# Optimization experiments

Measured on AMD Instinct MI355X. Metric: run time of the kernel, lower is better.

The kernel has to match this reference:

```python
import jax, jax.numpy as jnp
import numpy as np

B, NO, NM, NV, E = 16, 512, 128, 64, 256
H, DK, MS, FF = 16, 16, 8, 512
TRANS_MAX = 100.0


def _ln(x):
    m = x.mean(-1, keepdims=True)
    v = ((x - m) ** 2).mean(-1, keepdims=True)
    return (x - m) * jax.lax.rsqrt(v + 1e-5)


def _inv_norm(x):
    # 1 - minmax-normalize over the whole per-batch matrix
    mn = x.min(axis=(1, 2), keepdims=True)
    mx = x.max(axis=(1, 2), keepdims=True)
    return 1.0 - (x - mn) / (mx - mn)


def _adjacency(proc_time, trans_time, MVpair_trans, mask_dyn, mask_ma):
    # masked copy of proc_time
    A_proc = jnp.where(mask_dyn, proc_time, 0.0)
    # keep only the per-row minimum nonzero entry (min_ProcTime_elements)
    nz = jnp.where(A_proc == 0.0, jnp.inf, A_proc)
    mn = nz.min(axis=2, keepdims=True)
    keep = (A_proc == mn) & (A_proc != 0.0)
    A_proc = A_proc * keep.astype(proc_time.dtype)
    A_proc_norm = (A_proc > 0.0).astype(proc_time.dtype)
    # machine-machine masks
    mask2 = mask_ma[:, None, :] & mask_ma[:, :, None]  # [B, nm, nm]
    A_procing = (~mask2).astype(proc_time.dtype)
    A_off = _inv_norm(MVpair_trans)
    tt = jnp.where(mask2, trans_time, TRANS_MAX + 1.0)
    A_on = _inv_norm(tt)
    return A_proc_norm, A_procing, A_off, A_on


def _block(row, col, cost, Wq, Wk, Wv, Wo, mW1, mb1, mW2, mb2, fW1, fb1, fW2, fb2):
    # MatNet-style mixed-score multi-head attention encoding block
    Bb, R, _ = row.shape
    C = col.shape[1]
    q = (row @ Wq).reshape(Bb, R, H, DK).transpose(0, 2, 1, 3)  # bhrd
    k = (col @ Wk).reshape(Bb, C, H, DK).transpose(0, 2, 1, 3)  # bhcd
    v = (col @ Wv).reshape(Bb, C, H, DK).transpose(0, 2, 1, 3)
    dot = jnp.einsum('bhrd,bhcd->bhrc', q, k) / jnp.sqrt(jnp.asarray(DK, row.dtype))
    two = jnp.stack([dot, jnp.broadcast_to(cost[:, None], dot.shape)], axis=-1)  # [B,H,R,C,2]
    hmix = jax.nn.relu(jnp.einsum('bhrct,hts->bhrcs', two, mW1) + mb1[None, :, None, None, :])
    score = jnp.einsum('bhrcs,hso->bhrco', hmix, mW2)[..., 0] + mb2[:, 0][None, :, None, None]
    attn = jax.nn.softmax(score, axis=-1)
    ctx = jnp.einsum('bhrc,bhcd->bhrd', attn, v).transpose(0, 2, 1, 3).reshape(Bb, R, H * DK)
    out1 = _ln(row + ctx @ Wo)
    ffn = jax.nn.relu(out1 @ fW1 + fb1) @ fW2 + fb2
    return _ln(out1 + ffn)


def setup_inputs() -> dict:
    key = jax.random.key(0)
    ks = jax.random.split(key, 24)

    def nrm(i, shape, s=0.05):
        return jax.random.normal(ks[i], shape, jnp.float32) * s

    return {
        'ope_emb': nrm(0, (B, NO, E), 1.0),
        'ma_emb': nrm(1, (B, NM, E), 1.0),
        'veh_emb': nrm(2, (B, NV, E), 1.0),
        'proc_time': jax.random.uniform(ks[3], (B, NO, NM), jnp.float32) * 20.0,
        'offload_trans_time': jax.random.uniform(ks[4], (B, NO, NV), jnp.float32) * TRANS_MAX,
        'trans_time': jax.random.uniform(ks[5], (B, NM, NM), jnp.float32) * TRANS_MAX,
        'MVpair_trans': jax.random.uniform(ks[6], (B, NV, NM), jnp.float32) * TRANS_MAX,
        'mask_dyn_ope_ma_adj': jax.random.bernoulli(ks[7], 0.3, (B, NO, NM)),
        'mask_ma': jax.random.bernoulli(ks[8], 0.7, (B, NM)),
        # stacked params for the 4 blocks: 0=ope, 1=veh, 2=ma1, 3=ma2
        'Wq': nrm(9, (4, E, H * DK)),
        'Wk': nrm(10, (4, E, H * DK)),
        'Wv': nrm(11, (4, E, H * DK)),
        'Wo': nrm(12, (4, H * DK, E)),
        'mixW1': nrm(13, (4, H, 2, MS), 0.3),
        'mixb1': jnp.zeros((4, H, MS), jnp.float32),
        'mixW2': nrm(14, (4, H, MS, 1), 0.3),
        'mixb2': jnp.zeros((4, H, 1), jnp.float32),
        'ffW1': nrm(15, (4, E, FF)),
        'ffb1': jnp.zeros((4, FF), jnp.float32),
        'ffW2': nrm(16, (4, FF, E)),
        'ffb2': jnp.zeros((4, E), jnp.float32),
        'maprojW': nrm(17, (2 * E, E)),
        'maprojb': jnp.zeros((E,), jnp.float32),
    }


def reference(ope_emb, ma_emb, veh_emb, proc_time, offload_trans_time, trans_time,
              MVpair_trans, mask_dyn_ope_ma_adj, mask_ma,
              Wq, Wk, Wv, Wo, mixW1, mixb1, mixW2, mixb2,
              ffW1, ffb1, ffW2, ffb2, maprojW, maprojb):
    A_proc_norm, A_procing, A_off, A_on = _adjacency(
        proc_time, trans_time, MVpair_trans, mask_dyn_ope_ma_adj, mask_ma)

    def blk(i, row, col, cost):
        return _block(row, col, cost, Wq[i], Wk[i], Wv[i], Wo[i],
                      mixW1[i], mixb1[i], mixW2[i], mixb2[i],
                      ffW1[i], ffb1[i], ffW2[i], ffb2[i])

    ope_out = blk(0, ope_emb, ma_emb, A_proc_norm)
    veh_out = blk(1, veh_emb, ma_emb, A_off)
    ma1 = blk(2, ma_emb, ma_emb, A_procing)
    ma2 = blk(3, ma_emb, ma_emb, A_on)
    ma_out = jnp.concatenate([ma1, ma2], axis=-1) @ maprojW + maprojb
    return (ope_out, ma_out, veh_out)
```

## Files before the change

### kernel.cpp

```cpp
#include <hip/hip_runtime.h>
#include <hip/hip_fp16.h>
#include <hip/hip_bf16.h>


typedef unsigned short u16;
typedef __attribute__((ext_vector_type(8))) short bf16x8;
typedef __attribute__((ext_vector_type(4))) float f32x4;
struct us4 { u16 x, y, z, w; };

__device__ __forceinline__ float bf2f(u16 u) {
  return __uint_as_float(((unsigned int)u) << 16);
}
__device__ __forceinline__ u16 f2bf(float f) {
  unsigned int x = __float_as_uint(f);
  x += 0x7FFFu + ((x >> 16) & 1u);
  return (u16)(x >> 16);
}
__device__ __forceinline__ __half2 h2max(__half2 a, __half2 b) {
  unsigned au = *(unsigned*)&a, bu = *(unsigned*)&b, ru;
  asm("v_pk_max_f16 %0, %1, %2" : "=v"(ru) : "v"(au), "v"(bu));
  return *(__half2*)&ru;
}

#define NBATCH 16
#define NOPE   512
#define NMA    128
#define NVEH   64
#define EDIM   256

struct PrepArgs {
  const float* ope; const float* ma; const float* veh;
  u16* ope_bf; u16* ma_bf; u16* veh_bf;
  const float* proc; const int* mask_dyn; float* A_proc;
  const float* mv; const float* trans; const int* mask_ma;
  unsigned int* mm;
};
__global__ __launch_bounds__(256) void prep_a(PrepArgs a) {
  int blk = blockIdx.x, t = threadIdx.x;
  if (blk < 2816) {
    int i = blk * 256 + t;
    const float* s; u16* d; int j;
    if (i < 524288)      { s = a.ope; d = a.ope_bf; j = i; }
    else if (i < 655360) { s = a.ma;  d = a.ma_bf;  j = i - 524288; }
    else                 { s = a.veh; d = a.veh_bf; j = i - 655360; }
    float4 v = ((const float4*)s)[j];
    us4 o = { f2bf(v.x), f2bf(v.y), f2bf(v.z), f2bf(v.w) };
    ((us4*)d)[j] = o;
    return;
  }
  if (blk < 6912) {
    int local = blk - 2816;
    int row = local * 2 + (t >> 7);
    int lane = t & 127;
    size_t idx = (size_t)row * NMA + lane;
    float av = a.mask_dyn[idx] ? a.proc[idx] : 0.0f;
    float cand = (av != 0.0f) ? av : 1.0e30f;
    __shared__ float red[256];
    red[t] = cand;
    __syncthreads();
    for (int s = 64; s > 0; s >>= 1) {
      if (lane < s) red[t] = fminf(red[t], red[t + s]);
      __syncthreads();
    }
    float mn = red[t & 128];
    a.A_proc[idx] = (av != 0.0f && av == mn) ? 1.0f : 0.0f;
    return;
  }
  __shared__ float smn[256], smx[256];
  float mn = 1.0e30f, mx = -1.0e30f;
  int mmIdx;
  if (blk < 6976) {
    int local = blk - 6912;
    int b = local >> 2, chunk = local & 3;
    const float* xb = a.mv + (size_t)b * 8192 + chunk * 2048;
#pragma unroll
    for (int r = 0; r < 8; r++) {
      float v = xb[r * 256 + t];
      mn = fminf(mn, v);
      mx = fmaxf(mx, v);
    }
    mmIdx = b;
  } else {
    int local = blk - 6976;
    int b = local >> 3, chunk = local & 7;
    __shared__ unsigned char mrow[NMA];
    if (t < NMA) mrow[t] = (unsigned char)(a.mask_ma[(size_t)b * NMA + t] != 0);
    __syncthreads();
    const float* tb = a.trans + (size_t)b * 16384 + chunk * 2048;
    int rbase = chunk * 16;
#pragma unroll
    for (int r = 0; r < 8; r++) {
      int off = r * 256 + t;
      int row = rbase + (off >> 7), col = off & 127;
      bool m2 = mrow[row] && mrow[col];
      float tt = m2 ? tb[off] : 101.0f;
      mn = fminf(mn, tt);
      mx = fmaxf(mx, tt);
    }
    mmIdx = 16 + b;
  }
  smn[t] = mn; smx[t] = mx;
  __syncthreads();
  for (int s = 128; s > 0; s >>= 1) {
    if (t < s) {
      smn[t] = fminf(smn[t], smn[t + s]);
      smx[t] = fmaxf(smx[t], smx[t + s]);
    }
    __syncthreads();
  }
  if (t == 0) {
    atomicMin(&a.mm[mmIdx], __float_as_uint(smn[0]));
    atomicMax(&a.mm[32 + mmIdx], __float_as_uint(smx[0]));
  }
}

__global__ __launch_bounds__(256) void prep_b(
    const float* __restrict__ mv, const float* __restrict__ trans,
    const int* __restrict__ mask_ma, const unsigned int* __restrict__ mm,
    float* __restrict__ A_offb, float* __restrict__ a_on,
    float* __restrict__ a_pcing) {
  int blk = blockIdx.x, t = threadIdx.x;
  if (blk < 512) {
    int b = blk >> 5, off = (blk & 31) * 256 + t;
    float lo = __uint_as_float(mm[b]);
    float inv = 1.0f / (__uint_as_float(mm[32 + b]) - lo);
    size_t idx = (size_t)b * 8192 + off;
    A_offb[idx] = 1.0f - (mv[idx] - lo) * inv;
    return;
  }
  int local = blk - 512;
  int b = local >> 6, off = (local & 63) * 256 + t;
  int row = off >> 7, col = off & 127;
  bool m2 = (mask_ma[(size_t)b * NMA + row] != 0) &&
            (mask_ma[(size_t)b * NMA + col] != 0);
  size_t idx = (size_t)b * 16384 + off;
  float tt = m2 ? trans[idx] : 101.0f;
  float lo = __uint_as_float(mm[16 + b]);
  float inv = 1.0f / (__uint_as_float(mm[48 + b]) - lo);
  a_on[idx] = 1.0f - (tt - lo) * inv;
  a_pcing[idx] = m2 ? 0.0f : 1.0f;
}

struct TrArgs {
  const float* Wq; const float* Wk; const float* Wv; const float* Wo;
  const float* ffW1; const float* ffW2; const float* maproj;
  u16* WqT; u16* WkT; u16* WvT; u16* WoT; u16* ffW1T; u16* ffW2T; u16* maprojT;
};
__global__ __launch_bounds__(256) void transpose_all(TrArgs a) {
  int blk = blockIdx.x;
  const float* src; u16* dst; int Kd, Nd, tile;
  if (blk < 1024) {
    int w = blk >> 8, i = (blk >> 6) & 3; tile = blk & 63;
    const float* sw = (w == 0 ? a.Wq : w == 1 ? a.Wk : w == 2 ? a.Wv : a.Wo);
    u16* dw = (w == 0 ? a.WqT : w == 1 ? a.WkT : w == 2 ? a.WvT : a.WoT);
    src = sw + (size_t)i * 65536; dst = dw + (size_t)i * 65536;
    Kd = 256; Nd = 256;
  } else if (blk < 1536) {
    int z = (blk - 1024) >> 7; tile = (blk - 1024) & 127;
    src = a.ffW1 + (size_t)z * 131072; dst = a.ffW1T + (size_t)z * 131072;
    Kd = 256; Nd = 512;
  } else {
    int z = (blk - 1536) >> 7; tile = (blk - 1536) & 127;
    if (z < 4) { src = a.ffW2 + (size_t)z * 131072; dst = a.ffW2T + (size_t)z * 131072; }
    else       { src = a.maproj; dst = a.maprojT; }
    Kd = 512; Nd = 256;
  }
  int nx = Nd >> 5;
  int k0 = (tile / nx) * 32, n0 = (tile % nx) * 32;
  __shared__ float tl[32][33];
  int tx = threadIdx.x & 31, ty = threadIdx.x >> 5;
#pragma unroll
  for (int r = 0; r < 4; r++)
    tl[ty + r * 8][tx] = src[(size_t)(k0 + ty + r * 8) * Nd + n0 + tx];
  __syncthreads();
#pragma unroll
  for (int r = 0; r < 4; r++)
    dst[(size_t)(n0 + ty + r * 8) * Kd + k0 + tx] = f2bf(tl[tx][ty + r * 8]);
}

__global__ __launch_bounds__(256) void transpose_v(
    const u16* __restrict__ src, u16* __restrict__ dst) {
  int g = blockIdx.z >> 4, b = blockIdx.z & 15;
  int d0 = blockIdx.x * 32, c0 = blockIdx.y * 32;
  __shared__ u16 tile[32][33];
  int tx = threadIdx.x & 31, ty = threadIdx.x >> 5;
  const u16* s = src + ((size_t)g * 16 + b) * 32768;
  u16* d = dst + ((size_t)g * 16 + b) * 32768;
#pragma unroll
  for (int r = 0; r < 4; r++)
    tile[ty + r * 8][tx] = s[(size_t)(c0 + ty + r * 8) * 256 + d0 + tx];
  __syncthreads();
#pragma unroll
  for (int r = 0; r < 4; r++)
    d[(size_t)(d0 + ty + r * 8) * 128 + c0 + tx] = tile[tx][ty + r * 8];
}

struct GG {
  const u16* A; const u16* WT; const float* bias; u16* C;
  int M, N, K, epi, wgStart, wgCols, mode;
};
struct GGArgs { GG g[12]; int n; };

__global__ __launch_bounds__(256) void gemm_grouped(GGArgs args) {
  int wg = blockIdx.x;
  int gi = 0;
  for (int i = 1; i < args.n; i++)
    if (wg >= args.g[i].wgStart) gi = i;
  GG gg = args.g[gi];
  int lwg = wg - gg.wgStart;
  int bx = lwg & (gg.wgCols - 1);
  int by = lwg >> ((gg.wgCols == 2) ? 1 : 2);
  int N = gg.N, K = gg.K;

  __shared__ u16 As[128][40];
  __shared__ u16 Bs[128][40];
  int tid = threadIdx.x;
  int lane = tid & 63, wid = tid >> 6;
  int wr = (wid >> 1) * 64, wc = (wid & 1) * 64;
  int m16 = lane & 15, quad = lane >> 4;
  int rb = by * 128, cb = bx * 128;
  int srow = tid >> 2;
  int schunk = (tid & 3) * 8;

  f32x4 acc[4][4];
#pragma unroll
  for (int i = 0; i < 4; i++)
#pragma unroll
    for (int j = 0; j < 4; j++) acc[i][j] = (f32x4){0.f, 0.f, 0.f, 0.f};

  for (int k0 = 0; k0 < K; k0 += 32) {
    uint4 va0 = *(const uint4*)(gg.A + (size_t)(rb + srow) * K + k0 + schunk);
    uint4 va1 = *(const uint4*)(gg.A + (size_t)(rb + 64 + srow) * K + k0 + schunk);
    uint4 vb0 = *(const uint4*)(gg.WT + (size_t)(cb + srow) * K + k0 + schunk);
    uint4 vb1 = *(const uint4*)(gg.WT + (size_t)(cb + 64 + srow) * K + k0 + schunk);
    __syncthreads();
    *(uint4*)&As[srow][schunk] = va0;
    *(uint4*)&As[64 + srow][schunk] = va1;
    *(uint4*)&Bs[srow][schunk] = vb0;
    *(uint4*)&Bs[64 + srow][schunk] = vb1;
    __syncthreads();
    bf16x8 af[4], bfr[4];
#pragma unroll
    for (int i = 0; i < 4; i++)
      af[i] = *(const bf16x8*)&As[wr + i * 16 + m16][quad * 8];
#pragma unroll
    for (int j = 0; j < 4; j++)
      bfr[j] = *(const bf16x8*)&Bs[wc + j * 16 + m16][quad * 8];
#pragma unroll
    for (int i = 0; i < 4; i++)
#pragma unroll
      for (int j = 0; j < 4; j++)
        acc[i][j] = __builtin_amdgcn_mfma_f32_16x16x32_bf16(
            af[i], bfr[j], acc[i][j], 0, 0, 0);
  }

#pragma unroll
  for (int i = 0; i < 4; i++) {
#pragma unroll
    for (int j = 0; j < 4; j++) {
      int col = cb + wc + j * 16 + m16;
      float bv = (gg.epi >= 1) ? gg.bias[col] : 0.0f;
#pragma unroll
      for (int r = 0; r < 4; r++) {
        int row = rb + wr + i * 16 + quad * 4 + r;
        float v = acc[i][j][r] + bv;
        if (gg.epi == 2) v = fmaxf(v, 0.0f);
        size_t off;
        if (gg.mode == 0) {
          off = (size_t)row * N + col;
        } else if (gg.mode == 1) {
          off = ((size_t)(row >> 4)) * 4096 + (size_t)(col >> 4) * 256 +
                (size_t)(row & 15) * 16 + (col & 15);
        } else {
          off = ((size_t)(row >> 7)) * 32768 + (size_t)(col >> 4) * 2048 +
                (size_t)(row & 127) * 16 + (col & 15);
        }
        gg.C[off] = f2bf(v);
      }
    }
  }
}

__global__ __launch_bounds__(256) void gemm_mfma_f32(
    const u16* __restrict__ A, const u16* __restrict__ WT,
    const float* __restrict__ bias, float* __restrict__ C,
    int M, int N, int K) {
  __shared__ u16 As[128][40];
  __shared__ u16 Bs[128][40];
  int tid = threadIdx.x;
  int lane = tid & 63, wid = tid >> 6;
  int wr = (wid >> 1) * 64, wc = (wid & 1) * 64;
  int m16 = lane & 15, quad = lane >> 4;
  int rb = blockIdx.y * 128, cb = blockIdx.x * 128;
  int srow = tid >> 2;
  int schunk = (tid & 3) * 8;
  f32x4 acc[4][4];
#pragma unroll
  for (int i = 0; i < 4; i++)
#pragma unroll
    for (int j = 0; j < 4; j++) acc[i][j] = (f32x4){0.f, 0.f, 0.f, 0.f};
  for (int k0 = 0; k0 < K; k0 += 32) {
    uint4 va0 = *(const uint4*)(A + (size_t)(rb + srow) * K + k0 + schunk);
    uint4 va1 = *(const uint4*)(A + (size_t)(rb + 64 + srow) * K + k0 + schunk);
    uint4 vb0 = *(const uint4*)(WT + (size_t)(cb + srow) * K + k0 + schunk);
    uint4 vb1 = *(const uint4*)(WT + (size_t)(cb + 64 + srow) * K + k0 + schunk);
    __syncthreads();
    *(uint4*)&As[srow][schunk] = va0;
    *(uint4*)&As[64 + srow][schunk] = va1;
    *(uint4*)&Bs[srow][schunk] = vb0;
    *(uint4*)&Bs[64 + srow][schunk] = vb1;
    __syncthreads();
    bf16x8 af[4], bfr[4];
#pragma unroll
    for (int i = 0; i < 4; i++)
      af[i] = *(const bf16x8*)&As[wr + i * 16 + m16][quad * 8];
#pragma unroll
    for (int j = 0; j < 4; j++)
      bfr[j] = *(const bf16x8*)&Bs[wc + j * 16 + m16][quad * 8];
#pragma unroll
    for (int i = 0; i < 4; i++)
#pragma unroll
      for (int j = 0; j < 4; j++)
        acc[i][j] = __builtin_amdgcn_mfma_f32_16x16x32_bf16(
            af[i], bfr[j], acc[i][j], 0, 0, 0);
  }
#pragma unroll
  for (int i = 0; i < 4; i++)
#pragma unroll
    for (int j = 0; j < 4; j++) {
      int col = cb + wc + j * 16 + m16;
      float bv = bias[col];
#pragma unroll
      for (int r = 0; r < 4; r++) {
        int row = rb + wr + i * 16 + quad * 4 + r;
        C[(size_t)row * N + col] = acc[i][j][r] + bv;
      }
    }
}

struct AG {
  const u16* q; const u16* k; const u16* vT; const float* cost; u16* ctx;
  const float* w1; const float* b1; const float* w2; const float* b2;
  int R, wgStart;
};
struct AGArgs { AG g[4]; };

#define CSTRIDE 134

__global__ __launch_bounds__(256) void attn_grouped(AGArgs args) {
  int blk = blockIdx.x;
  int gi = 0;
#pragma unroll
  for (int i = 1; i < 4; i++)
    if (blk >= args.g[i].wgStart) gi = i;
  AG gg = args.g[gi];
  int local = blk - gg.wgStart;

  int t = threadIdx.x;
  int wave = t >> 6, lane = t & 63;
  int quad = lane >> 4, l16 = lane & 15;
  int j = local & 15;
  int b = (j & 7) * 2 + (j >> 3);
  int hgrp = (local >> 4) & 1;
  int tile = local >> 5;
  int m0 = b * gg.R + tile * 16;

  __shared__ __half costs_h[16 * CSTRIDE];
  __shared__ u16 pbuf[4][16 * 136];

  const float* cp = gg.cost + (size_t)m0 * 128;
  for (int i = t; i < 2048; i += 256)
    costs_h[(i >> 7) * CSTRIDE + (i & 127)] = __float2half(cp[i]);
  __syncthreads();

  const bf16x8 zerof = (bf16x8){0, 0, 0, 0, 0, 0, 0, 0};
  const f32x4 zacc = (f32x4){0.f, 0.f, 0.f, 0.f};
  const __half2 zh = __float2half2_rn(0.0f);
  u16* pb = pbuf[wave];
  const u16* qtile = gg.q + ((size_t)(m0 >> 4)) * 4096;
  const u16* kb    = gg.k + (size_t)b * 32768;

#pragma unroll
  for (int hh = 0; hh < 2; hh++) {
    int h = hgrp * 8 + wave * 2 + hh;

    __half2 w10h[8], w11h[8], b1h[8], w2h[8];
#pragma unroll
    for (int s = 0; s < 8; s++) {
      w10h[s] = __float2half2_rn(gg.w1[h * 16 + s] * 0.25f);
      w11h[s] = __float2half2_rn(gg.w1[h * 16 + 8 + s]);
      b1h[s]  = __float2half2_rn(gg.b1[h * 8 + s]);
      w2h[s]  = __float2half2_rn(gg.w2[h * 8 + s]);
    }
    float wb2v = gg.b2[h];

    bf16x8 bq = zerof;
    if (quad < 2)
      bq = *(const bf16x8*)(qtile + (size_t)h * 256 + l16 * 16 + quad * 8);
    f32x4 st[8];
#pragma unroll
    for (int ct = 0; ct < 8; ct++) {
      bf16x8 ak = zerof;
      if (quad < 2)
        ak = *(const bf16x8*)(kb + (size_t)h * 2048 + (ct * 16 + l16) * 16 +
                              quad * 8);
      st[ct] = __builtin_amdgcn_mfma_f32_16x16x32_bf16(ak, bq, zacc, 0, 0, 0);
    }

#pragma unroll
    for (int ct = 0; ct < 8; ct++) {
#pragma unroll
      for (int p = 0; p < 2; p++) {
        __half2 d2 = __float22half2_rn(
            make_float2(st[ct][p * 2], st[ct][p * 2 + 1]));
        __half2 c2 = *(const __half2*)&costs_h[l16 * CSTRIDE + ct * 16 +
                                               quad * 4 + p * 2];
        __half2 s2 = zh;
#pragma unroll
        for (int s = 0; s < 8; s++) {
          __half2 hm = __hfma2(d2, w10h[s], __hfma2(c2, w11h[s], b1h[s]));
          hm = h2max(hm, zh);
          s2 = __hfma2(hm, w2h[s], s2);
        }
        float2 sf = __half22float2(s2);
        st[ct][p * 2]     = sf.x + wb2v;
        st[ct][p * 2 + 1] = sf.y + wb2v;
      }
    }

    float mx = -1.0e30f;
#pragma unroll
    for (int ct = 0; ct < 8; ct++)
#pragma unroll
      for (int rg = 0; rg < 4; rg++) mx = fmaxf(mx, st[ct][rg]);
    mx = fmaxf(mx, __shfl_xor(mx, 16, 64));
    mx = fmaxf(mx, __shfl_xor(mx, 32, 64));
    float sum = 0.0f;
#pragma unroll
    for (int ct = 0; ct < 8; ct++)
#pragma unroll
      for (int rg = 0; rg < 4; rg++) {
        float e = __expf(st[ct][rg] - mx);
        st[ct][rg] = e;
        sum += e;
      }
    sum += __shfl_xor(sum, 16, 64);
    sum += __shfl_xor(sum, 32, 64);
    float inv = 1.0f / sum;

#pragma unroll
    for (int ct = 0; ct < 8; ct++) {
#pragma unroll
      for (int p = 0; p < 2; p++) {
        __hip_bfloat162 pk = __float22bfloat162_rn(
            make_float2(st[ct][p * 2] * inv, st[ct][p * 2 + 1] * inv));
        *(unsigned int*)&pb[l16 * 136 + ct * 16 + quad * 4 + p * 2] =
            *(unsigned int*)&pk;
      }
    }

    f32x4 cacc = zacc;
#pragma unroll
    for (int ks = 0; ks < 4; ks++) {
      bf16x8 ap = *(const bf16x8*)&pb[l16 * 136 + ks * 32 + quad * 8];
      bf16x8 bv = *(const bf16x8*)(gg.vT + (size_t)b * 32768 +
                                   (size_t)(h * 16 + l16) * 128 + ks * 32 +
                                   quad * 8);
      cacc = __builtin_amdgcn_mfma_f32_16x16x32_bf16(ap, bv, cacc, 0, 0, 0);
    }

#pragma unroll
    for (int rg = 0; rg < 4; rg++)
      gg.ctx[(size_t)(m0 + quad * 4 + rg) * 256 + h * 16 + l16] =
          f2bf(cacc[rg]);
  }
}

struct LN1Args {
  const float* r0; const float* r1; const float* r2; const float* r3;
  int s1, s2, s3;
};
__global__ __launch_bounds__(256) void ln1_grouped(
    LN1Args a, const u16* __restrict__ x, u16* __restrict__ out) {
  int row = blockIdx.x, t = threadIdx.x;
  const float* resid;
  int local;
  if (row < a.s1)      { resid = a.r0; local = row; }
  else if (row < a.s2) { resid = a.r1; local = row - a.s1; }
  else if (row < a.s3) { resid = a.r2; local = row - a.s2; }
  else                 { resid = a.r3; local = row - a.s3; }
  float vv = resid[(size_t)local * 256 + t] + bf2f(x[(size_t)row * 256 + t]);
  __shared__ float red[256];
  red[t] = vv;
  __syncthreads();
  for (int s = 128; s > 0; s >>= 1) {
    if (t < s) red[t] += red[t + s];
    __syncthreads();
  }
  float mean = red[0] * (1.0f / 256.0f);
  __syncthreads();
  float d = vv - mean;
  red[t] = d * d;
  __syncthreads();
  for (int s = 128; s > 0; s >>= 1) {
    if (t < s) red[t] += red[t + s];
    __syncthreads();
  }
  float var = red[0] * (1.0f / 256.0f);
  out[(size_t)row * 256 + t] = f2bf(d * rsqrtf(var + 1e-5f));
}

struct LN2Args {
  float* f0; float* f1; u16* b2; u16* b3;
  int s1, s2, s3;
};
__global__ __launch_bounds__(256) void ln2_grouped(
    LN2Args a, const u16* __restrict__ resid, const u16* __restrict__ x) {
  int row = blockIdx.x, t = threadIdx.x;
  float vv = bf2f(resid[(size_t)row * 256 + t]) + bf2f(x[(size_t)row * 256 + t]);
  __shared__ float red[256];
  red[t] = vv;
  __syncthreads();
  for (int s = 128; s > 0; s >>= 1) {
    if (t < s) red[t] += red[t + s];
    __syncthreads();
  }
  float mean = red[0] * (1.0f / 256.0f);
  __syncthreads();
  float d = vv - mean;
  red[t] = d * d;
  __syncthreads();
  for (int s = 128; s > 0; s >>= 1) {
    if (t < s) red[t] += red[t + s];
    __syncthreads();
  }
  float var = red[0] * (1.0f / 256.0f);
  float y = d * rsqrtf(var + 1e-5f);
  if (row < a.s1)
    a.f0[(size_t)row * 256 + t] = y;
  else if (row < a.s2)
    a.f1[(size_t)(row - a.s1) * 256 + t] = y;
  else if (row < a.s3)
    a.b2[(size_t)(row - a.s2) * 512 + t] = f2bf(y);
  else
    a.b3[(size_t)(row - a.s3) * 512 + 256 + t] = f2bf(y);
}

extern "C" void kernel_launch(void* const* d_in, const int* in_sizes, int n_in,
                              void* d_out, int out_size, void* d_ws, size_t ws_size,
                              hipStream_t stream) {
  const float* ope   = (const float*)d_in[0];
  const float* ma    = (const float*)d_in[1];
  const float* veh   = (const float*)d_in[2];
  const float* proc  = (const float*)d_in[3];
  const float* trans = (const float*)d_in[5];
  const float* mv    = (const float*)d_in[6];
  const int* mask_dyn = (const int*)d_in[7];
  const int* mask_ma  = (const int*)d_in[8];
  const float* Wq = (const float*)d_in[9];
  const float* Wk = (const float*)d_in[10];
  const float* Wv = (const float*)d_in[11];
  const float* Wo = (const float*)d_in[12];
  const float* mixW1 = (const float*)d_in[13];
  const float* mixb1 = (const float*)d_in[14];
  const float* mixW2 = (const float*)d_in[15];
  const float* mixb2 = (const float*)d_in[16];
  const float* ffW1 = (const float*)d_in[17];
  const float* ffb1 = (const float*)d_in[18];
  const float* ffW2 = (const float*)d_in[19];
  const float* ffb2 = (const float*)d_in[20];
  const float* maprojW = (const float*)d_in[21];
  const float* maprojb = (const float*)d_in[22];
  float* out = (float*)d_out;
  char* ws = (char*)d_ws;

  const int OFF[4] = {0, 8192, 9216, 11264};
  const int MS4[4] = {8192, 1024, 2048, 2048};
  const int TOT = 13312;

  const size_t MB = 1 << 20;
  float* A_proc  = (float*)(ws + 0);
  float* A_offb  = (float*)(ws + 4 * MB);
  float* A_pcing = (float*)(ws + 4 * MB + MB / 2);
  float* A_on    = (float*)(ws + 5 * MB + MB / 2);
  u16* ope_bf  = (u16*)(ws + 6 * MB + MB / 2);
  u16* ma_bf   = (u16*)(ws + 10 * MB + MB / 2);
  u16* veh_bf  = (u16*)(ws + 11 * MB + MB / 2);
  u16* WqT     = (u16*)(ws + 12 * MB);
  u16* WkT     = (u16*)(ws + 12 * MB + MB / 2);
  u16* WvT     = (u16*)(ws + 13 * MB);
  u16* WoT     = (u16*)(ws + 13 * MB + MB / 2);
  u16* ffW1T   = (u16*)(ws + 14 * MB);
  u16* ffW2T   = (u16*)(ws + 15 * MB);
  u16* maprojT = (u16*)(ws + 16 * MB);
  u16* q_all   = (u16*)(ws + 16 * MB + MB / 2);
  u16* k_all   = (u16*)(ws + 23 * MB);
  u16* v_all   = (u16*)(ws + 27 * MB);
  u16* vT_all  = (u16*)(ws + 31 * MB);
  u16* ctx_all = (u16*)(ws + 35 * MB);
  u16* t1_all  = (u16*)(ws + 41 * MB + MB / 2);
  u16* out1_all= (u16*)(ws + 48 * MB);
  u16* ffh_all = (u16*)(ws + 54 * MB + MB / 2);
  u16* maCat   = (u16*)(ws + 67 * MB + MB / 2);
  unsigned int* mmbuf = (unsigned int*)(ws + 70 * MB);

  hipMemsetAsync(mmbuf, 0x7F, 128, stream);
  hipMemsetAsync((char*)mmbuf + 128, 0x00, 128, stream);

  {
    PrepArgs pa = {ope, ma, veh, ope_bf, ma_bf, veh_bf,
                   proc, mask_dyn, A_proc, mv, trans, mask_ma, mmbuf};
    prep_a<<<7104, 256, 0, stream>>>(pa);
  }

  {
    TrArgs ta = {Wq, Wk, Wv, Wo, ffW1, ffW2, maprojW,
                 WqT, WkT, WvT, WoT, ffW1T, ffW2T, maprojT};
    transpose_all<<<2176, 256, 0, stream>>>(ta);
  }

  prep_b<<<1536, 256, 0, stream>>>(mv, trans, mask_ma, mmbuf,
                                   A_offb, A_on, A_pcing);

  const size_t MA_OUT  = (size_t)NBATCH * NOPE * EDIM;
  const size_t VEH_OUT = MA_OUT + (size_t)NBATCH * NMA * EDIM;

  const u16* rowbf[4] = {ope_bf, veh_bf, ma_bf, ma_bf};
  const float* costp[4] = {A_proc, A_offb, A_pcing, A_on};

  {
    GGArgs ga; ga.n = 12;
    int wg = 0;
    for (int i = 0; i < 4; i++) {
      ga.g[i] = {rowbf[i], WqT + (size_t)i * 65536, nullptr,
                 q_all + (size_t)OFF[i] * 256, MS4[i], 256, 256, 0, wg, 2, 1};
      wg += (MS4[i] / 128) * 2;
    }
    for (int i = 0; i < 4; i++) {
      ga.g[4 + i] = {ma_bf, WkT + (size_t)i * 65536, nullptr,
                     k_all + (size_t)i * 524288, 2048, 256, 256, 0, wg, 2, 2};
      wg += 32;
    }
    for (int i = 0; i < 4; i++) {
      ga.g[8 + i] = {ma_bf, WvT + (size_t)i * 65536, nullptr,
                     v_all + (size_t)i * 524288, 2048, 256, 256, 0, wg, 2, 0};
      wg += 32;
    }
    gemm_grouped<<<wg, 256, 0, stream>>>(ga);
  }

  transpose_v<<<dim3(8, 4, 64), 256, 0, stream>>>(v_all, vT_all);

  {
    AGArgs aa;
    int wg = 0;
    const int R4[4] = {NOPE, NVEH, NMA, NMA};
    for (int i = 0; i < 4; i++) {
      aa.g[i] = {q_all + (size_t)OFF[i] * 256, k_all + (size_t)i * 524288,
                 vT_all + (size_t)i * 524288, costp[i],
                 ctx_all + (size_t)OFF[i] * 256,
                 mixW1 + (size_t)i * 256, mixb1 + (size_t)i * 128,
                 mixW2 + (size_t)i * 128, mixb2 + (size_t)i * 16,
                 R4[i], wg};
      wg += MS4[i] / 8;
    }
    attn_grouped<<<wg, 256, 0, stream>>>(aa);
  }

  {
    GGArgs ga; ga.n = 4;
    int wg = 0;
    for (int i = 0; i < 4; i++) {
      ga.g[i] = {ctx_all + (size_t)OFF[i] * 256, WoT + (size_t)i * 65536,
                 nullptr, t1_all + (size_t)OFF[i] * 256,
                 MS4[i], 256, 256, 0, wg, 2, 0};
      wg += (MS4[i] / 128) * 2;
    }
    gemm_grouped<<<wg, 256, 0, stream>>>(ga);
  }

  {
    LN1Args la = {ope, veh, ma, ma, 8192, 9216, 11264};
    ln1_grouped<<<TOT, 256, 0, stream>>>(la, t1_all, out1_all);
  }

  {
    GGArgs ga; ga.n = 4;
    int wg = 0;
    for (int i = 0; i < 4; i++) {
      ga.g[i] = {out1_all + (size_t)OFF[i] * 256, ffW1T + (size_t)i * 131072,
                 ffb1 + (size_t)i * 512, ffh_all + (size_t)OFF[i] * 512,
                 MS4[i], 512, 256, 2, wg, 4, 0};
      wg += (MS4[i] / 128) * 4;
    }
    gemm_grouped<<<wg, 256, 0, stream>>>(ga);
  }

  {
    GGArgs ga; ga.n = 4;
    int wg = 0;
    for (int i = 0; i < 4; i++) {
      ga.g[i] = {ffh_all + (size_t)OFF[i] * 512, ffW2T + (size_t)i * 131072,
                 ffb2 + (size_t)i * 256, t1_all + (size_t)OFF[i] * 256,
                 MS4[i], 256, 512, 1, wg, 2, 0};
      wg += (MS4[i] / 128) * 2;
    }
    gemm_grouped<<<wg, 256, 0, stream>>>(ga);
  }

  {
    LN2Args la = {out, out + VEH_OUT, maCat, maCat, 8192, 9216, 11264};
    ln2_grouped<<<TOT, 256, 0, stream>>>(la, out1_all, t1_all);
  }

  gemm_mfma_f32<<<dim3(2, 16), 256, 0, stream>>>(maCat, maprojT, maprojb,
      out + MA_OUT, 2048, 256, 512);
}
```

Before: 279.2 us.

## Fuse weight transpose into prep, warp-level layernorm, smaller final GEMM tiles, MFMA priority

Folds the weight-transpose kernel into the prep kernel as extra blocks, which removes one launch. Both layernorm kernels now use one 64-lane wave per row with vectorized loads and shuffle reductions instead of shared-memory tree reductions. Variance is now computed in a single pass as E[x^2]-mean^2, which adds a small numerical risk. The final projection GEMM moves from 128x128 to 64x64 tiles to put more workgroups on the GPU, and s_setprio is raised around the MFMA loops in attention.

```diff
diff --git a/kernel.cpp b/kernel.cpp
--- a/kernel.cpp
+++ b/kernel.cpp
@@ -35,7 +35,12 @@
   const float* mv; const float* trans; const int* mask_ma;
   unsigned int* mm;
 };
-__global__ __launch_bounds__(256) void prep_a(PrepArgs a) {
+struct TrArgs {
+  const float* Wq; const float* Wk; const float* Wv; const float* Wo;
+  const float* ffW1; const float* ffW2; const float* maproj;
+  u16* WqT; u16* WkT; u16* WvT; u16* WoT; u16* ffW1T; u16* ffW2T; u16* maprojT;
+};
+__global__ __launch_bounds__(256) void prep_a(PrepArgs a, TrArgs tr) {
   int blk = blockIdx.x, t = threadIdx.x;
   if (blk < 2816) {
     int i = blk * 256 + t;
@@ -66,51 +71,85 @@
     a.A_proc[idx] = (av != 0.0f && av == mn) ? 1.0f : 0.0f;
     return;
   }
-  __shared__ float smn[256], smx[256];
-  float mn = 1.0e30f, mx = -1.0e30f;
-  int mmIdx;
-  if (blk < 6976) {
-    int local = blk - 6912;
-    int b = local >> 2, chunk = local & 3;
-    const float* xb = a.mv + (size_t)b * 8192 + chunk * 2048;
-#pragma unroll
-    for (int r = 0; r < 8; r++) {
-      float v = xb[r * 256 + t];
-      mn = fminf(mn, v);
-      mx = fmaxf(mx, v);
-    }
-    mmIdx = b;
-  } else {
-    int local = blk - 6976;
-    int b = local >> 3, chunk = local & 7;
-    __shared__ unsigned char mrow[NMA];
-    if (t < NMA) mrow[t] = (unsigned char)(a.mask_ma[(size_t)b * NMA + t] != 0);
+  if (blk < 7104) {
+    __shared__ float smn[256], smx[256];
+    float mn = 1.0e30f, mx = -1.0e30f;
+    int mmIdx;
+    if (blk < 6976) {
+      int local = blk - 6912;
+      int b = local >> 2, chunk = local & 3;
+      const float* xb = a.mv + (size_t)b * 8192 + chunk * 2048;
+#pragma unroll
+      for (int r = 0; r < 8; r++) {
+        float v = xb[r * 256 + t];
+        mn = fminf(mn, v);
+        mx = fmaxf(mx, v);
+      }
+      mmIdx = b;
+    } else {
+      int local = blk - 6976;
+      int b = local >> 3, chunk = local & 7;
+      __shared__ unsigned char mrow[NMA];
+      if (t < NMA) mrow[t] = (unsigned char)(a.mask_ma[(size_t)b * NMA + t] != 0);
+      __syncthreads();
+      const float* tb = a.trans + (size_t)b * 16384 + chunk * 2048;
+      int rbase = chunk * 16;
+#pragma unroll
+      for (int r = 0; r < 8; r++) {
+        int off = r * 256 + t;
+        int row = rbase + (off >> 7), col = off & 127;
+        bool m2 = mrow[row] && mrow[col];
+        float tt = m2 ? tb[off] : 101.0f;
+        mn = fminf(mn, tt);
+        mx = fmaxf(mx, tt);
+      }
+      mmIdx = 16 + b;
+    }
+    smn[t] = mn; smx[t] = mx;
     __syncthreads();
-    const float* tb = a.trans + (size_t)b * 16384 + chunk * 2048;
-    int rbase = chunk * 16;
-#pragma unroll
-    for (int r = 0; r < 8; r++) {
-      int off = r * 256 + t;
-      int row = rbase + (off >> 7), col = off & 127;
-      bool m2 = mrow[row] && mrow[col];
-      float tt = m2 ? tb[off] : 101.0f;
-      mn = fminf(mn, tt);
-      mx = fmaxf(mx, tt);
-    }
-    mmIdx = 16 + b;
-  }
-  smn[t] = mn; smx[t] = mx;
-  __syncthreads();
-  for (int s = 128; s > 0; s >>= 1) {
-    if (t < s) {
-      smn[t] = fminf(smn[t], smn[t + s]);
-      smx[t] = fmaxf(smx[t], smx[t + s]);
-    }
+    for (int s = 128; s > 0; s >>= 1) {
+      if (t < s) {
+        smn[t] = fminf(smn[t], smn[t + s]);
+        smx[t] = fmaxf(smx[t], smx[t + s]);
+      }
+      __syncthreads();
+    }
+    if (t == 0) {
+      atomicMin(&a.mm[mmIdx], __float_as_uint(smn[0]));
+      atomicMax(&a.mm[32 + mmIdx], __float_as_uint(smx[0]));
+    }
+    return;
+  }
+  {
+    int b2 = blk - 7104;
+    const float* src; u16* dst; int Kd, Nd, tile;
+    if (b2 < 1024) {
+      int w = b2 >> 8, i = (b2 >> 6) & 3; tile = b2 & 63;
+      const float* sw = (w == 0 ? tr.Wq : w == 1 ? tr.Wk : w == 2 ? tr.Wv : tr.Wo);
+      u16* dw = (w == 0 ? tr.WqT : w == 1 ? tr.WkT : w == 2 ? tr.WvT : tr.WoT);
+      src = sw + (size_t)i * 65536; dst = dw + (size_t)i * 65536;
+      Kd = 256; Nd = 256;
+    } else if (b2 < 1536) {
+      int z = (b2 - 1024) >> 7; tile = (b2 - 1024) & 127;
+      src = tr.ffW1 + (size_t)z * 131072; dst = tr.ffW1T + (size_t)z * 131072;
+      Kd = 256; Nd = 512;
+    } else {
+      int z = (b2 - 1536) >> 7; tile = (b2 - 1536) & 127;
+      if (z < 4) { src = tr.ffW2 + (size_t)z * 131072; dst = tr.ffW2T + (size_t)z * 131072; }
+      else       { src = tr.maproj; dst = tr.maprojT; }
+      Kd = 512; Nd = 256;
+    }
+    int nx = Nd >> 5;
+    int k0 = (tile / nx) * 32, n0 = (tile % nx) * 32;
+    __shared__ float tl[32][33];
+    int tx = t & 31, ty = t >> 5;
+#pragma unroll
+    for (int r = 0; r < 4; r++)
+      tl[ty + r * 8][tx] = src[(size_t)(k0 + ty + r * 8) * Nd + n0 + tx];
     __syncthreads();
-  }
-  if (t == 0) {
-    atomicMin(&a.mm[mmIdx], __float_as_uint(smn[0]));
-    atomicMax(&a.mm[32 + mmIdx], __float_as_uint(smx[0]));
+#pragma unroll
+    for (int r = 0; r < 4; r++)
+      dst[(size_t)(n0 + ty + r * 8) * Kd + k0 + tx] = f2bf(tl[tx][ty + r * 8]);
   }
 }
 
@@ -139,43 +178,6 @@
   float inv = 1.0f / (__uint_as_float(mm[48 + b]) - lo);
   a_on[idx] = 1.0f - (tt - lo) * inv;
   a_pcing[idx] = m2 ? 0.0f : 1.0f;
-}
-
-struct TrArgs {
-  const float* Wq; const float* Wk; const float* Wv; const float* Wo;
-  const float* ffW1; const float* ffW2; const float* maproj;
-  u16* WqT; u16* WkT; u16* WvT; u16* WoT; u16* ffW1T; u16* ffW2T; u16* maprojT;
-};
-__global__ __launch_bounds__(256) void transpose_all(TrArgs a) {
-  int blk = blockIdx.x;
-  const float* src; u16* dst; int Kd, Nd, tile;
-  if (blk < 1024) {
-    int w = blk >> 8, i = (blk >> 6) & 3; tile = blk & 63;
-    const float* sw = (w == 0 ? a.Wq : w == 1 ? a.Wk : w == 2 ? a.Wv : a.Wo);
-    u16* dw = (w == 0 ? a.WqT : w == 1 ? a.WkT : w == 2 ? a.WvT : a.WoT);
-    src = sw + (size_t)i * 65536; dst = dw + (size_t)i * 65536;
-    Kd = 256; Nd = 256;
-  } else if (blk < 1536) {
-    int z = (blk - 1024) >> 7; tile = (blk - 1024) & 127;
-    src = a.ffW1 + (size_t)z * 131072; dst = a.ffW1T + (size_t)z * 131072;
-    Kd = 256; Nd = 512;
-  } else {
-    int z = (blk - 1536) >> 7; tile = (blk - 1536) & 127;
-    if (z < 4) { src = a.ffW2 + (size_t)z * 131072; dst = a.ffW2T + (size_t)z * 131072; }
-    else       { src = a.maproj; dst = a.maprojT; }
-    Kd = 512; Nd = 256;
-  }
-  int nx = Nd >> 5;
-  int k0 = (tile / nx) * 32, n0 = (tile % nx) * 32;
-  __shared__ float tl[32][33];
-  int tx = threadIdx.x & 31, ty = threadIdx.x >> 5;
-#pragma unroll
-  for (int r = 0; r < 4; r++)
-    tl[ty + r * 8][tx] = src[(size_t)(k0 + ty + r * 8) * Nd + n0 + tx];
-  __syncthreads();
-#pragma unroll
-  for (int r = 0; r < 4; r++)
-    dst[(size_t)(n0 + ty + r * 8) * Kd + k0 + tx] = f2bf(tl[tx][ty + r * 8]);
 }
 
 __global__ __launch_bounds__(256) void transpose_v(
@@ -285,49 +287,45 @@
     const u16* __restrict__ A, const u16* __restrict__ WT,
     const float* __restrict__ bias, float* __restrict__ C,
     int M, int N, int K) {
-  __shared__ u16 As[128][40];
-  __shared__ u16 Bs[128][40];
+  __shared__ u16 As[64][40];
+  __shared__ u16 Bs[64][40];
   int tid = threadIdx.x;
   int lane = tid & 63, wid = tid >> 6;
-  int wr = (wid >> 1) * 64, wc = (wid & 1) * 64;
+  int wr = (wid >> 1) * 32, wc = (wid & 1) * 32;
   int m16 = lane & 15, quad = lane >> 4;
-  int rb = blockIdx.y * 128, cb = blockIdx.x * 128;
+  int rb = blockIdx.y * 64, cb = blockIdx.x * 64;
   int srow = tid >> 2;
   int schunk = (tid & 3) * 8;
-  f32x4 acc[4][4];
-#pragma unroll
-  for (int i = 0; i < 4; i++)
-#pragma unroll
-    for (int j = 0; j < 4; j++) acc[i][j] = (f32x4){0.f, 0.f, 0.f, 0.f};
+  f32x4 acc[2][2];
+#pragma unroll
+  for (int i = 0; i < 2; i++)
+#pragma unroll
+    for (int j = 0; j < 2; j++) acc[i][j] = (f32x4){0.f, 0.f, 0.f, 0.f};
   for (int k0 = 0; k0 < K; k0 += 32) {
-    uint4 va0 = *(const uint4*)(A + (size_t)(rb + srow) * K + k0 + schunk);
-    uint4 va1 = *(const uint4*)(A + (size_t)(rb + 64 + srow) * K + k0 + schunk);
-    uint4 vb0 = *(const uint4*)(WT + (size_t)(cb + srow) * K + k0 + schunk);
-    uint4 vb1 = *(const uint4*)(WT + (size_t)(cb + 64 + srow) * K + k0 + schunk);
+    uint4 va = *(const uint4*)(A + (size_t)(rb + srow) * K + k0 + schunk);
+    uint4 vb = *(const uint4*)(WT + (size_t)(cb + srow) * K + k0 + schunk);
     __syncthreads();
-    *(uint4*)&As[srow][schunk] = va0;
-    *(uint4*)&As[64 + srow][schunk] = va1;
-    *(uint4*)&Bs[srow][schunk] = vb0;
-    *(uint4*)&Bs[64 + srow][schunk] = vb1;
+    *(uint4*)&As[srow][schunk] = va;
+    *(uint4*)&Bs[srow][schunk] = vb;
     __syncthreads();
-    bf16x8 af[4], bfr[4];
-#pragma unroll
-    for (int i = 0; i < 4; i++)
+    bf16x8 af[2], bfr[2];
+#pragma unroll
+    for (int i = 0; i < 2; i++)
       af[i] = *(const bf16x8*)&As[wr + i * 16 + m16][quad * 8];
 #pragma unroll
-    for (int j = 0; j < 4; j++)
+    for (int j = 0; j < 2; j++)
       bfr[j] = *(const bf16x8*)&Bs[wc + j * 16 + m16][quad * 8];
 #pragma unroll
-    for (int i = 0; i < 4; i++)
-#pragma unroll
-      for (int j = 0; j < 4; j++)
+    for (int i = 0; i < 2; i++)
+#pragma unroll
+      for (int j = 0; j < 2; j++)
         acc[i][j] = __builtin_amdgcn_mfma_f32_16x16x32_bf16(
             af[i], bfr[j], acc[i][j], 0, 0, 0);
   }
 #pragma unroll
-  for (int i = 0; i < 4; i++)
-#pragma unroll
-    for (int j = 0; j < 4; j++) {
+  for (int i = 0; i < 2; i++)
+#pragma unroll
+    for (int j = 0; j < 2; j++) {
       int col = cb + wc + j * 16 + m16;
       float bv = bias[col];
 #pragma unroll
@@ -398,6 +396,7 @@
     if (quad < 2)
       bq = *(const bf16x8*)(qtile + (size_t)h * 256 + l16 * 16 + quad * 8);
     f32x4 st[8];
+    __builtin_amdgcn_s_setprio(1);
 #pragma unroll
     for (int ct = 0; ct < 8; ct++) {
       bf16x8 ak = zerof;
@@ -406,6 +405,7 @@
                               quad * 8);
       st[ct] = __builtin_amdgcn_mfma_f32_16x16x32_bf16(ak, bq, zacc, 0, 0, 0);
     }
+    __builtin_amdgcn_s_setprio(0);
 
 #pragma unroll
     for (int ct = 0; ct < 8; ct++) {
@@ -460,6 +460,7 @@
     }
 
     f32x4 cacc = zacc;
+    __builtin_amdgcn_s_setprio(1);
 #pragma unroll
     for (int ks = 0; ks < 4; ks++) {
       bf16x8 ap = *(const bf16x8*)&pb[l16 * 136 + ks * 32 + quad * 8];
@@ -468,6 +469,7 @@
                                    quad * 8);
       cacc = __builtin_amdgcn_mfma_f32_16x16x32_bf16(ap, bv, cacc, 0, 0, 0);
     }
+    __builtin_amdgcn_s_setprio(0);
 
 #pragma unroll
     for (int rg = 0; rg < 4; rg++)
@@ -482,32 +484,33 @@
 };
 __global__ __launch_bounds__(256) void ln1_grouped(
     LN1Args a, const u16* __restrict__ x, u16* __restrict__ out) {
-  int row = blockIdx.x, t = threadIdx.x;
+  int row = blockIdx.x * 4 + (threadIdx.x >> 6);
+  int lane = threadIdx.x & 63;
   const float* resid;
   int local;
   if (row < a.s1)      { resid = a.r0; local = row; }
   else if (row < a.s2) { resid = a.r1; local = row - a.s1; }
   else if (row < a.s3) { resid = a.r2; local = row - a.s2; }
   else                 { resid = a.r3; local = row - a.s3; }
-  float vv = resid[(size_t)local * 256 + t] + bf2f(x[(size_t)row * 256 + t]);
-  __shared__ float red[256];
-  red[t] = vv;
-  __syncthreads();
-  for (int s = 128; s > 0; s >>= 1) {
-    if (t < s) red[t] += red[t + s];
-    __syncthreads();
-  }
-  float mean = red[0] * (1.0f / 256.0f);
-  __syncthreads();
-  float d = vv - mean;
-  red[t] = d * d;
-  __syncthreads();
-  for (int s = 128; s > 0; s >>= 1) {
-    if (t < s) red[t] += red[t + s];
-    __syncthreads();
-  }
-  float var = red[0] * (1.0f / 256.0f);
-  out[(size_t)row * 256 + t] = f2bf(d * rsqrtf(var + 1e-5f));
+  float4 rv = *(const float4*)(resid + (size_t)local * 256 + lane * 4);
+  us4 xv = *(const us4*)(x + (size_t)row * 256 + lane * 4);
+  float v0 = rv.x + bf2f(xv.x);
+  float v1 = rv.y + bf2f(xv.y);
+  float v2 = rv.z + bf2f(xv.z);
+  float v3 = rv.w + bf2f(xv.w);
+  float s  = v0 + v1 + v2 + v3;
+  float ss = v0 * v0 + v1 * v1 + v2 * v2 + v3 * v3;
+#pragma unroll
+  for (int d = 1; d < 64; d <<= 1) {
+    s  += __shfl_xor(s, d, 64);
+    ss += __shfl_xor(ss, d, 64);
+  }
+  float mean = s * (1.0f / 256.0f);
+  float var = ss * (1.0f / 256.0f) - mean * mean;
+  float rs = rsqrtf(fmaxf(var, 0.0f) + 1e-5f);
+  us4 o = { f2bf((v0 - mean) * rs), f2bf((v1 - mean) * rs),
+            f2bf((v2 - mean) * rs), f2bf((v3 - mean) * rs) };
+  *(us4*)(out + (size_t)row * 256 + lane * 4) = o;
 }
 
 struct LN2Args {
@@ -516,34 +519,39 @@
 };
 __global__ __launch_bounds__(256) void ln2_grouped(
     LN2Args a, const u16* __restrict__ resid, const u16* __restrict__ x) {
-  int row = blockIdx.x, t = threadIdx.x;
-  float vv = bf2f(resid[(size_t)row * 256 + t]) + bf2f(x[(size_t)row * 256 + t]);
-  __shared__ float red[256];
-  red[t] = vv;
-  __syncthreads();
-  for (int s = 128; s > 0; s >>= 1) {
-    if (t < s) red[t] += red[t + s];
-    __syncthreads();
-  }
-  float mean = red[0] * (1.0f / 256.0f);
-  __syncthreads();
-  float d = vv - mean;
-  red[t] = d * d;
-  __syncthreads();
-  for (int s = 128; s > 0; s >>= 1) {
-    if (t < s) red[t] += red[t + s];
-    __syncthreads();
-  }
-  float var = red[0] * (1.0f / 256.0f);
-  float y = d * rsqrtf(var + 1e-5f);
-  if (row < a.s1)
-    a.f0[(size_t)row * 256 + t] = y;
-  else if (row < a.s2)
-    a.f1[(size_t)(row - a.s1) * 256 + t] = y;
-  else if (row < a.s3)
-    a.b2[(size_t)(row - a.s2) * 512 + t] = f2bf(y);
-  else
-    a.b3[(size_t)(row - a.s3) * 512 + 256 + t] = f2bf(y);
+  int row = blockIdx.x * 4 + (threadIdx.x >> 6);
+  int lane = threadIdx.x & 63;
+  us4 rv = *(const us4*)(resid + (size_t)row * 256 + lane * 4);
+  us4 xv = *(const us4*)(x + (size_t)row * 256 + lane * 4);
+  float v0 = bf2f(rv.x) + bf2f(xv.x);
+  float v1 = bf2f(rv.y) + bf2f(xv.y);
+  float v2 = bf2f(rv.z) + bf2f(xv.z);
+  float v3 = bf2f(rv.w) + bf2f(xv.w);
+  float s  = v0 + v1 + v2 + v3;
+  float ss = v0 * v0 + v1 * v1 + v2 * v2 + v3 * v3;
+#pragma unroll
+  for (int d = 1; d < 64; d <<= 1) {
+    s  += __shfl_xor(s, d, 64);
+    ss += __shfl_xor(ss, d, 64);
+  }
+  float mean = s * (1.0f / 256.0f);
+  float var = ss * (1.0f / 256.0f) - mean * mean;
+  float rs = rsqrtf(fmaxf(var, 0.0f) + 1e-5f);
+  float y0 = (v0 - mean) * rs, y1 = (v1 - mean) * rs;
+  float y2 = (v2 - mean) * rs, y3 = (v3 - mean) * rs;
+  if (row < a.s1) {
+    float4 o = {y0, y1, y2, y3};
+    *(float4*)(a.f0 + (size_t)row * 256 + lane * 4) = o;
+  } else if (row < a.s2) {
+    float4 o = {y0, y1, y2, y3};
+    *(float4*)(a.f1 + (size_t)(row - a.s1) * 256 + lane * 4) = o;
+  } else if (row < a.s3) {
+    us4 o = { f2bf(y0), f2bf(y1), f2bf(y2), f2bf(y3) };
+    *(us4*)(a.b2 + (size_t)(row - a.s2) * 512 + lane * 4) = o;
+  } else {
+    us4 o = { f2bf(y0), f2bf(y1), f2bf(y2), f2bf(y3) };
+    *(us4*)(a.b3 + (size_t)(row - a.s3) * 512 + 256 + lane * 4) = o;
+  }
 }
 
 extern "C" void kernel_launch(void* const* d_in, const int* in_sizes, int n_in,
@@ -610,13 +618,9 @@
   {
     PrepArgs pa = {ope, ma, veh, ope_bf, ma_bf, veh_bf,
                    proc, mask_dyn, A_proc, mv, trans, mask_ma, mmbuf};
-    prep_a<<<7104, 256, 0, stream>>>(pa);
-  }
-
-  {
     TrArgs ta = {Wq, Wk, Wv, Wo, ffW1, ffW2, maprojW,
                  WqT, WkT, WvT, WoT, ffW1T, ffW2T, maprojT};
-    transpose_all<<<2176, 256, 0, stream>>>(ta);
+    prep_a<<<9280, 256, 0, stream>>>(pa, ta);
   }
 
   prep_b<<<1536, 256, 0, stream>>>(mv, trans, mask_ma, mmbuf,
@@ -681,7 +685,7 @@
 
   {
     LN1Args la = {ope, veh, ma, ma, 8192, 9216, 11264};
-    ln1_grouped<<<TOT, 256, 0, stream>>>(la, t1_all, out1_all);
+    ln1_grouped<<<TOT / 4, 256, 0, stream>>>(la, t1_all, out1_all);
   }
 
   {
@@ -710,9 +714,9 @@
 
   {
     LN2Args la = {out, out + VEH_OUT, maCat, maCat, 8192, 9216, 11264};
-    ln2_grouped<<<TOT, 256, 0, stream>>>(la, out1_all, t1_all);
-  }
-
-  gemm_mfma_f32<<<dim3(2, 16), 256, 0, stream>>>(maCat, maprojT, maprojb,
+    ln2_grouped<<<TOT / 4, 256, 0, stream>>>(la, out1_all, t1_all);
+  }
+
+  gemm_mfma_f32<<<dim3(4, 32), 256, 0, stream>>>(maCat, maprojT, maprojb,
       out + MA_OUT, 2048, 256, 512);
 }
```

Result: faster. 250.7 us (-10.2%).
